# Optimization experiments

Hardware: AMD Instinct MI355X
Metric: run time of the kernel (lower is better)

Reference implementation:

```python
import jax, jax.numpy as jnp
import numpy as np

N, IN_DIM, HEADS, C = 100000, 128, 4, 32  # out_dim = HEADS*C = 128
E = 1600000


def setup_inputs() -> dict:
    key = jax.random.key(0)
    ks = jax.random.split(key, 9)
    x = jax.random.normal(ks[0], (N, IN_DIM), dtype=jnp.float32)
    edge_index = jax.random.randint(ks[1], (2, E), 0, N, dtype=jnp.int64)
    # GATConv params
    W = jax.random.normal(ks[2], (HEADS * C, IN_DIM), dtype=jnp.float32) * (1.0 / np.sqrt(IN_DIM))
    att_src = jax.random.normal(ks[3], (HEADS, C), dtype=jnp.float32) * 0.1
    att_dst = jax.random.normal(ks[4], (HEADS, C), dtype=jnp.float32) * 0.1
    bias = jax.random.normal(ks[5], (HEADS * C,), dtype=jnp.float32) * 0.01
    # complex phase + LayerNorm params
    phase = jax.random.normal(ks[6], (HEADS * C,), dtype=jnp.float32) * 0.02
    gamma = 1.0 + jax.random.normal(ks[7], (HEADS * C,), dtype=jnp.float32) * 0.01
    beta = jax.random.normal(ks[8], (HEADS * C,), dtype=jnp.float32) * 0.01
    return {"x": x, "edge_index": edge_index, "W": W, "att_src": att_src,
            "att_dst": att_dst, "bias": bias, "phase": phase, "gamma": gamma, "beta": beta}


def reference(x, edge_index, W, att_src, att_dst, bias, phase, gamma, beta):
    src, dst = edge_index[0], edge_index[1]
    h = (x @ W.T).reshape(N, HEADS, C)                      # [N,H,C]
    a_src = jnp.einsum('nhc,hc->nh', h, att_src)            # [N,H]
    a_dst = jnp.einsum('nhc,hc->nh', h, att_dst)
    e = jax.nn.leaky_relu(a_src[src] + a_dst[dst], 0.2)     # [E,H]
    # segment softmax over destination nodes (numerically stable)
    m = jax.ops.segment_max(e, dst, num_segments=N)         # [N,H]
    ex = jnp.exp(e - m[dst])
    s = jax.ops.segment_sum(ex, dst, num_segments=N)        # [N,H]
    alpha = ex / (s[dst] + 1e-16)                           # [E,H]
    msg = h[src] * alpha[:, :, None]                        # [E,H,C]
    out = jax.ops.segment_sum(msg, dst, num_segments=N).reshape(N, HEADS * C) + bias
    # complex phase magnitude: sqrt((h cos p)^2 + (h sin p)^2 + eps)
    mag = jnp.sqrt((out * jnp.cos(phase)) ** 2 + (out * jnp.sin(phase)) ** 2 + 1e-12)
    # LayerNorm
    mu = mag.mean(-1, keepdims=True)
    var = ((mag - mu) ** 2).mean(-1, keepdims=True)
    hn = (mag - mu) / jnp.sqrt(var + 1e-5) * gamma + beta
    return jax.nn.gelu(hn, approximate=False)
```

## Files before the change

### kernel.cpp

```cpp
#include <hip/hip_runtime.h>
#include <hip/hip_bf16.h>

#define N_ 100000
#define E_ 1600000
#define D_ 128
#define H_ 4
#define C_ 32
#define CAP 64
#define XSTR 136
#define NBUILD 256
#define NLIN 512

using bf16 = __hip_bfloat16;
typedef __attribute__((ext_vector_type(8))) short short8;
typedef __attribute__((ext_vector_type(4))) float f32x4;
typedef __attribute__((ext_vector_type(2))) float f32x2;

__device__ __forceinline__ float u2f(unsigned u) { return __uint_as_float(u); }
__device__ __forceinline__ unsigned short f2bu(float v) {
  bf16 t = __float2bfloat16(v);
  return *(unsigned short*)&t;
}

__global__ __launch_bounds__(256) void k_build_linear(
    const float* __restrict__ x, const float* __restrict__ W,
    const float* __restrict__ att_src, const float* __restrict__ att_dst,
    const int* __restrict__ ei, int* __restrict__ cnt, int* __restrict__ slot,
    bf16* __restrict__ h, float* __restrict__ a_src, float* __restrict__ a_dst) {
  __shared__ unsigned short WB[16384];
  __shared__ unsigned short XS[64 * XSTR];
  __shared__ float ats[128], atd[128];
  const int tid = threadIdx.x;
  const int bid = blockIdx.x;
  const int role = bid % 3;

  if (role == 0) {
    const int bb = bid / 3;
    for (int base = bb * 2048; base < E_; base += NBUILD * 2048) {
      int d[8], s[8];
      bool live[8];
#pragma unroll
      for (int k = 0; k < 8; k++) {
        const int e = base + k * 256 + tid;
        live[k] = e < E_;
        d[k] = 0; s[k] = 0;
        if (live[k]) { d[k] = ei[E_ + e]; s[k] = ei[e]; }
      }
#pragma unroll
      for (int k = 0; k < 8; k++) {
        if (live[k]) {
          const int p = atomicAdd(&cnt[d[k]], 1);
          if (p < CAP) slot[d[k] * CAP + p] = s[k];
        }
      }
    }
    return;
  }

  const int lb = (bid / 3) * 2 + (role - 1);
  const int lane = tid & 63, w = tid >> 6;
  const int n15 = lane & 15, quad = lane >> 4;

  for (int i = tid; i < 16384; i += 256) {
    const int n = i >> 7, k = i & 127;
    const int kk = k >> 5, q = (k >> 3) & 3, j = k & 7;
    const int frag = kk * 8 + (n >> 4);
    WB[frag * 512 + q * 128 + (n & 15) * 8 + j] = f2bu(W[n * 128 + k]);
  }
  if (tid < 128) { ats[tid] = att_src[tid]; atd[tid] = att_dst[tid]; }
  __syncthreads();

  const int nrb = (N_ + 63) / 64;
  for (int rb = lb; rb < nrb; rb += NLIN) {
    const int row0 = rb * 64;
    const int arow = row0 + w * 16 + n15;

    short8 af[4];
#pragma unroll
    for (int kk = 0; kk < 4; kk++) {
      float4 p = make_float4(0.f, 0.f, 0.f, 0.f);
      float4 q = make_float4(0.f, 0.f, 0.f, 0.f);
      if (arow < N_) {
        const float* xp = &x[(size_t)arow * 128 + kk * 32 + quad * 8];
        p = *(const float4*)xp;
        q = *(const float4*)(xp + 4);
      }
      short8 a;
      a[0] = f2bu(p.x); a[1] = f2bu(p.y); a[2] = f2bu(p.z); a[3] = f2bu(p.w);
      a[4] = f2bu(q.x); a[5] = f2bu(q.y); a[6] = f2bu(q.z); a[7] = f2bu(q.w);
      af[kk] = a;
    }

    f32x4 acc[8] = {};
#pragma unroll
    for (int kk = 0; kk < 4; kk++)
#pragma unroll
      for (int t = 0; t < 8; t++) {
        const short8 b = *(const short8*)&WB[(kk * 8 + t) * 512 + lane * 8];
        acc[t] = __builtin_amdgcn_mfma_f32_16x16x32_bf16(af[kk], b, acc[t], 0, 0, 0);
      }

#pragma unroll
    for (int t = 0; t < 8; t++)
#pragma unroll
      for (int reg = 0; reg < 4; reg++)
        XS[(w * 16 + quad * 4 + reg) * XSTR + t * 16 + n15] = f2bu(acc[t][reg]);

    const int lrow = lane >> 2, hd = lane & 3, cb = hd * 32;
    const int grow = row0 + w * 16 + lrow;
    if (grow < N_) {
      float ps = 0.f, pd = 0.f;
#pragma unroll
      for (int g = 0; g < 4; g++) {
        const uint4 v = *(const uint4*)&XS[(w * 16 + lrow) * XSTR + cb + g * 8];
        *(uint4*)&h[(size_t)grow * 128 + cb + g * 8] = v;
        const unsigned uu[4] = {v.x, v.y, v.z, v.w};
#pragma unroll
        for (int p2 = 0; p2 < 4; p2++) {
          const float f0 = u2f(uu[p2] << 16);
          const float f1 = u2f(uu[p2] & 0xffff0000u);
          const int cc = cb + g * 8 + p2 * 2;
          ps = fmaf(f0, ats[cc], ps);  ps = fmaf(f1, ats[cc + 1], ps);
          pd = fmaf(f0, atd[cc], pd);  pd = fmaf(f1, atd[cc + 1], pd);
        }
      }
      a_src[grow * 4 + hd] = ps;
      a_dst[grow * 4 + hd] = pd;
    }
  }
}

__global__ __launch_bounds__(256) void k_gather(
    const int* __restrict__ cnt, const int* __restrict__ slot,
    const float* __restrict__ a_src, const float* __restrict__ a_dst,
    const bf16* __restrict__ h, const float* __restrict__ bias,
    const float* __restrict__ gamma, const float* __restrict__ beta,
    float* __restrict__ out) {
  const int lane = threadIdx.x & 63;
  const int d = blockIdx.x * 4 + (threadIdx.x >> 6);
  if (d >= N_) return;
  const int head = lane >> 4;
  const int ch = lane * 2;
  const int deg0 = cnt[d];
  const int deg = deg0 < CAP ? deg0 : CAP;
  const float ad = a_dst[d * 4 + head];
  const int* __restrict__ srow = slot + (size_t)d * CAP;

  int my_src = 0;
  if (lane < deg) my_src = srow[lane];

  float acc0 = 0.f, acc1 = 0.f, sumw = 0.f;

  int j = 0;
  for (; j + 8 <= deg; j += 8) {
    int ss[8];
#pragma unroll
    for (int k = 0; k < 8; k++) ss[k] = __builtin_amdgcn_readlane(my_src, j + k);
    float as[8];
#pragma unroll
    for (int k = 0; k < 8; k++) as[k] = a_src[ss[k] * 4 + head];
    unsigned hh[8];
#pragma unroll
    for (int k = 0; k < 8; k++) hh[k] = *(const unsigned*)&h[((size_t)ss[k] << 7) + ch];
#pragma unroll
    for (int k = 0; k < 8; k++) {
      float ev = as[k] + ad;
      ev = (ev > 0.f) ? ev : 0.2f * ev;
      const float wv = __expf(ev);
      sumw += wv;
      acc0 = fmaf(wv, u2f(hh[k] << 16), acc0);
      acc1 = fmaf(wv, u2f(hh[k] & 0xffff0000u), acc1);
    }
  }
  for (; j + 4 <= deg; j += 4) {
    int ss[4];
#pragma unroll
    for (int k = 0; k < 4; k++) ss[k] = __builtin_amdgcn_readlane(my_src, j + k);
    float as[4];
#pragma unroll
    for (int k = 0; k < 4; k++) as[k] = a_src[ss[k] * 4 + head];
    unsigned hh[4];
#pragma unroll
    for (int k = 0; k < 4; k++) hh[k] = *(const unsigned*)&h[((size_t)ss[k] << 7) + ch];
#pragma unroll
    for (int k = 0; k < 4; k++) {
      float ev = as[k] + ad;
      ev = (ev > 0.f) ? ev : 0.2f * ev;
      const float wv = __expf(ev);
      sumw += wv;
      acc0 = fmaf(wv, u2f(hh[k] << 16), acc0);
      acc1 = fmaf(wv, u2f(hh[k] & 0xffff0000u), acc1);
    }
  }
  for (; j < deg; ++j) {
    const int s = __builtin_amdgcn_readlane(my_src, j);
    const float as = a_src[s * 4 + head];
    const unsigned hv = *(const unsigned*)&h[((size_t)s << 7) + ch];
    float ev = as + ad;
    ev = (ev > 0.f) ? ev : 0.2f * ev;
    const float wv = __expf(ev);
    sumw += wv;
    acc0 = fmaf(wv, u2f(hv << 16), acc0);
    acc1 = fmaf(wv, u2f(hv & 0xffff0000u), acc1);
  }

  const float inv = 1.0f / (sumw + 1e-16f);
  const float2 bi = *(const float2*)&bias[ch];
  const float v0 = acc0 * inv + bi.x;
  const float v1 = acc1 * inv + bi.y;
  const float m0i = sqrtf(v0 * v0 + 1e-12f);
  const float m1i = sqrtf(v1 * v1 + 1e-12f);

  float s1r = m0i + m1i;
#pragma unroll
  for (int off = 32; off > 0; off >>= 1) s1r += __shfl_xor(s1r, off);
  const float mu = s1r * (1.0f / 128.0f);
  const float d0 = m0i - mu, d1 = m1i - mu;
  float q = d0 * d0 + d1 * d1;
#pragma unroll
  for (int off = 32; off > 0; off >>= 1) q += __shfl_xor(q, off);
  const float rstd = rsqrtf(q * (1.0f / 128.0f) + 1e-5f);
  const float2 ga = *(const float2*)&gamma[ch];
  const float2 be = *(const float2*)&beta[ch];
  const float hn0 = d0 * rstd * ga.x + be.x;
  const float hn1 = d1 * rstd * ga.y + be.y;
  const float g0 = 0.5f * hn0 * (1.0f + erff(hn0 * 0.70710678118654752f));
  const float g1 = 0.5f * hn1 * (1.0f + erff(hn1 * 0.70710678118654752f));
  f32x2 gv; gv.x = g0; gv.y = g1;
  __builtin_nontemporal_store(gv, (f32x2*)&out[(size_t)d * 128 + ch]);
}

extern "C" void kernel_launch(void* const* d_in, const int* in_sizes, int n_in,
                              void* d_out, int out_size, void* d_ws, size_t ws_size,
                              hipStream_t stream) {
  const float* x       = (const float*)d_in[0];
  const int*   ei      = (const int*)d_in[1];
  const float* W       = (const float*)d_in[2];
  const float* att_src = (const float*)d_in[3];
  const float* att_dst = (const float*)d_in[4];
  const float* bias    = (const float*)d_in[5];
  const float* gamma   = (const float*)d_in[7];
  const float* beta    = (const float*)d_in[8];
  float* out = (float*)d_out;

  bf16*  h     = (bf16*)d_ws;
  float* a_src = (float*)(h + (size_t)N_ * D_);
  float* a_dst = a_src + (size_t)N_ * H_;
  int*   cnt   = (int*)(a_dst + (size_t)N_ * H_);
  int*   slot  = cnt + (size_t)N_;

  (void)hipMemsetAsync(cnt, 0, (size_t)N_ * sizeof(int), stream);

  k_build_linear<<<768, 256, 0, stream>>>(x, W, att_src, att_dst, ei, cnt,
                                          slot, h, a_src, a_dst);
  k_gather<<<(N_ + 3) / 4, 256, 0, stream>>>(cnt, slot, a_src, a_dst, h,
                                             bias, gamma, beta, out);
}
```

Before: 300.0 us.

## Replace per-node atomic slot lists with partitioned counting-sort CSR build

Replaces the global per-destination atomicAdd into fixed 64-slot lists with a two-level counting sort. Edges are histogrammed into 782 partitions of 128 nodes, scanned, and scattered with LDS atomics into packed (src, local dst) words. Each gather block then sorts its partition's edges in shared memory and handles 128 nodes, four waves doing 32 each. This removes the contended global atomics and the slot array, but adds two kernel launches, a single-block serial scan, and a fixed EBUF cap that silently truncates partitions with more than 2560 edges (about 2048 on average).

```diff
diff --git a/kernel.cpp b/kernel.cpp
--- a/kernel.cpp
+++ b/kernel.cpp
@@ -6,10 +6,13 @@
 #define D_ 128
 #define H_ 4
 #define C_ 32
-#define CAP 64
 #define XSTR 136
-#define NBUILD 256
-#define NLIN 512
+#define NSCAT 128
+#define E_CHUNK 12500
+#define PARTS 782
+#define NP 128
+#define EBUF 2560
+#define NLIN 640
 
 using bf16 = __hip_bfloat16;
 typedef __attribute__((ext_vector_type(8))) short short8;
@@ -22,42 +25,78 @@
   return *(unsigned short*)&t;
 }
 
-__global__ __launch_bounds__(256) void k_build_linear(
+__global__ __launch_bounds__(256) void k_histo(const int* __restrict__ ei,
+                                               int* __restrict__ count) {
+  __shared__ int hist[PARTS];
+  const int b = blockIdx.x, tid = threadIdx.x;
+  for (int i = tid; i < PARTS; i += 256) hist[i] = 0;
+  __syncthreads();
+  const int base = b * E_CHUNK;
+  for (int i = tid; i < E_CHUNK; i += 256) {
+    const int d = ei[E_ + base + i];
+    atomicAdd(&hist[d >> 7], 1);
+  }
+  __syncthreads();
+  for (int p = tid; p < PARTS; p += 256) count[p * NSCAT + b] = hist[p];
+}
+
+__global__ __launch_bounds__(1024) void k_scan(int* __restrict__ count,
+                                               int* __restrict__ part_ptr) {
+  __shared__ int ps[1024];
+  const int p = threadIdx.x;
+  int sum = 0;
+  if (p < PARTS)
+    for (int b = 0; b < NSCAT; b++) sum += count[p * NSCAT + b];
+  ps[p] = (p < PARTS) ? sum : 0;
+  __syncthreads();
+  for (int off = 1; off < 1024; off <<= 1) {
+    const int v = (p >= off) ? ps[p - off] : 0;
+    __syncthreads();
+    ps[p] += v;
+    __syncthreads();
+  }
+  if (p < PARTS) {
+    const int excl = ps[p] - sum;
+    part_ptr[p] = excl;
+    int run = excl;
+    for (int b = 0; b < NSCAT; b++) {
+      const int c = count[p * NSCAT + b];
+      count[p * NSCAT + b] = run;
+      run += c;
+    }
+  }
+  if (p == 0) part_ptr[PARTS] = E_;
+}
+
+__global__ __launch_bounds__(256) void k_scatter_linear(
     const float* __restrict__ x, const float* __restrict__ W,
     const float* __restrict__ att_src, const float* __restrict__ att_dst,
-    const int* __restrict__ ei, int* __restrict__ cnt, int* __restrict__ slot,
-    bf16* __restrict__ h, float* __restrict__ a_src, float* __restrict__ a_dst) {
+    const int* __restrict__ ei, const int* __restrict__ base,
+    int* __restrict__ eout, bf16* __restrict__ h,
+    float* __restrict__ a_src, float* __restrict__ a_dst) {
   __shared__ unsigned short WB[16384];
   __shared__ unsigned short XS[64 * XSTR];
   __shared__ float ats[128], atd[128];
   const int tid = threadIdx.x;
   const int bid = blockIdx.x;
-  const int role = bid % 3;
-
-  if (role == 0) {
-    const int bb = bid / 3;
-    for (int base = bb * 2048; base < E_; base += NBUILD * 2048) {
-      int d[8], s[8];
-      bool live[8];
-#pragma unroll
-      for (int k = 0; k < 8; k++) {
-        const int e = base + k * 256 + tid;
-        live[k] = e < E_;
-        d[k] = 0; s[k] = 0;
-        if (live[k]) { d[k] = ei[E_ + e]; s[k] = ei[e]; }
-      }
-#pragma unroll
-      for (int k = 0; k < 8; k++) {
-        if (live[k]) {
-          const int p = atomicAdd(&cnt[d[k]], 1);
-          if (p < CAP) slot[d[k] * CAP + p] = s[k];
-        }
-      }
+
+  if (bid < NSCAT) {
+    int* lbase = (int*)WB;
+    const int b = bid;
+    for (int p = tid; p < PARTS; p += 256) lbase[p] = base[p * NSCAT + b];
+    __syncthreads();
+    const int ebase = b * E_CHUNK;
+    for (int i = tid; i < E_CHUNK; i += 256) {
+      const int e = ebase + i;
+      const int s = ei[e];
+      const int d = ei[E_ + e];
+      const int pos = atomicAdd(&lbase[d >> 7], 1);
+      eout[pos] = s | ((d & 127) << 20);
     }
     return;
   }
 
-  const int lb = (bid / 3) * 2 + (role - 1);
+  const int lb = bid - NSCAT;
   const int lane = tid & 63, w = tid >> 6;
   const int n15 = lane & 15, quad = lane >> 4;
 
@@ -96,8 +135,8 @@
     for (int kk = 0; kk < 4; kk++)
 #pragma unroll
       for (int t = 0; t < 8; t++) {
-        const short8 b = *(const short8*)&WB[(kk * 8 + t) * 512 + lane * 8];
-        acc[t] = __builtin_amdgcn_mfma_f32_16x16x32_bf16(af[kk], b, acc[t], 0, 0, 0);
+        const short8 bfr = *(const short8*)&WB[(kk * 8 + t) * 512 + lane * 8];
+        acc[t] = __builtin_amdgcn_mfma_f32_16x16x32_bf16(af[kk], bfr, acc[t], 0, 0, 0);
       }
 
 #pragma unroll
@@ -131,103 +170,113 @@
 }
 
 __global__ __launch_bounds__(256) void k_gather(
-    const int* __restrict__ cnt, const int* __restrict__ slot,
+    const int* __restrict__ part_ptr, const int* __restrict__ eout,
     const float* __restrict__ a_src, const float* __restrict__ a_dst,
     const bf16* __restrict__ h, const float* __restrict__ bias,
     const float* __restrict__ gamma, const float* __restrict__ beta,
     float* __restrict__ out) {
-  const int lane = threadIdx.x & 63;
-  const int d = blockIdx.x * 4 + (threadIdx.x >> 6);
-  if (d >= N_) return;
+  __shared__ int ebuf[EBUF];
+  __shared__ int lsrc[EBUF];
+  __shared__ int lcnt[NP], loff[NP], lptr[NP], ls[NP];
+  const int p = blockIdx.x, tid = threadIdx.x;
+  const int lo = part_ptr[p];
+  int ne = part_ptr[p + 1] - lo;
+  if (ne > EBUF) ne = EBUF;
+
+  for (int i = tid; i < ne; i += 256) ebuf[i] = eout[lo + i];
+  for (int n = tid; n < NP; n += 256) { lcnt[n] = 0; loff[n] = 0; }
+  __syncthreads();
+  for (int i = tid; i < ne; i += 256) atomicAdd(&lcnt[ebuf[i] >> 20], 1);
+  __syncthreads();
+  if (tid < NP) ls[tid] = lcnt[tid];
+  __syncthreads();
+  for (int off = 1; off < NP; off <<= 1) {
+    const int v = (tid < NP && tid >= off) ? ls[tid - off] : 0;
+    __syncthreads();
+    if (tid < NP) ls[tid] += v;
+    __syncthreads();
+  }
+  if (tid < NP) lptr[tid] = ls[tid] - lcnt[tid];
+  __syncthreads();
+  for (int i = tid; i < ne; i += 256) {
+    const int v = ebuf[i];
+    const int n = v >> 20;
+    const int off = atomicAdd(&loff[n], 1);
+    lsrc[lptr[n] + off] = v & 0x1FFFF;
+  }
+  __syncthreads();
+
+  const int lane = tid & 63, wid = tid >> 6;
   const int head = lane >> 4;
   const int ch = lane * 2;
-  const int deg0 = cnt[d];
-  const int deg = deg0 < CAP ? deg0 : CAP;
-  const float ad = a_dst[d * 4 + head];
-  const int* __restrict__ srow = slot + (size_t)d * CAP;
-
-  int my_src = 0;
-  if (lane < deg) my_src = srow[lane];
-
-  float acc0 = 0.f, acc1 = 0.f, sumw = 0.f;
-
-  int j = 0;
-  for (; j + 8 <= deg; j += 8) {
-    int ss[8];
-#pragma unroll
-    for (int k = 0; k < 8; k++) ss[k] = __builtin_amdgcn_readlane(my_src, j + k);
-    float as[8];
-#pragma unroll
-    for (int k = 0; k < 8; k++) as[k] = a_src[ss[k] * 4 + head];
-    unsigned hh[8];
-#pragma unroll
-    for (int k = 0; k < 8; k++) hh[k] = *(const unsigned*)&h[((size_t)ss[k] << 7) + ch];
-#pragma unroll
-    for (int k = 0; k < 8; k++) {
-      float ev = as[k] + ad;
+
+  for (int nn = 0; nn < 32; nn++) {
+    const int n = wid * 32 + nn;
+    const int g = p * NP + n;
+    if (g >= N_) break;
+    const int deg = lcnt[n];
+    const int p0 = lptr[n];
+    const float ad = a_dst[g * 4 + head];
+    float acc0 = 0.f, acc1 = 0.f, sumw = 0.f;
+
+    int j = 0;
+    for (; j + 8 <= deg; j += 8) {
+      int ss[8];
+#pragma unroll
+      for (int k = 0; k < 8; k++) ss[k] = lsrc[p0 + j + k];
+      float as[8];
+#pragma unroll
+      for (int k = 0; k < 8; k++) as[k] = a_src[ss[k] * 4 + head];
+      unsigned hh[8];
+#pragma unroll
+      for (int k = 0; k < 8; k++) hh[k] = *(const unsigned*)&h[((size_t)ss[k] << 7) + ch];
+#pragma unroll
+      for (int k = 0; k < 8; k++) {
+        float ev = as[k] + ad;
+        ev = (ev > 0.f) ? ev : 0.2f * ev;
+        const float wv = __expf(ev);
+        sumw += wv;
+        acc0 = fmaf(wv, u2f(hh[k] << 16), acc0);
+        acc1 = fmaf(wv, u2f(hh[k] & 0xffff0000u), acc1);
+      }
+    }
+    for (; j < deg; ++j) {
+      const int s = lsrc[p0 + j];
+      const float as = a_src[s * 4 + head];
+      const unsigned hv = *(const unsigned*)&h[((size_t)s << 7) + ch];
+      float ev = as + ad;
       ev = (ev > 0.f) ? ev : 0.2f * ev;
       const float wv = __expf(ev);
       sumw += wv;
-      acc0 = fmaf(wv, u2f(hh[k] << 16), acc0);
-      acc1 = fmaf(wv, u2f(hh[k] & 0xffff0000u), acc1);
-    }
-  }
-  for (; j + 4 <= deg; j += 4) {
-    int ss[4];
-#pragma unroll
-    for (int k = 0; k < 4; k++) ss[k] = __builtin_amdgcn_readlane(my_src, j + k);
-    float as[4];
-#pragma unroll
-    for (int k = 0; k < 4; k++) as[k] = a_src[ss[k] * 4 + head];
-    unsigned hh[4];
-#pragma unroll
-    for (int k = 0; k < 4; k++) hh[k] = *(const unsigned*)&h[((size_t)ss[k] << 7) + ch];
-#pragma unroll
-    for (int k = 0; k < 4; k++) {
-      float ev = as[k] + ad;
-      ev = (ev > 0.f) ? ev : 0.2f * ev;
-      const float wv = __expf(ev);
-      sumw += wv;
-      acc0 = fmaf(wv, u2f(hh[k] << 16), acc0);
-      acc1 = fmaf(wv, u2f(hh[k] & 0xffff0000u), acc1);
-    }
-  }
-  for (; j < deg; ++j) {
-    const int s = __builtin_amdgcn_readlane(my_src, j);
-    const float as = a_src[s * 4 + head];
-    const unsigned hv = *(const unsigned*)&h[((size_t)s << 7) + ch];
-    float ev = as + ad;
-    ev = (ev > 0.f) ? ev : 0.2f * ev;
-    const float wv = __expf(ev);
-    sumw += wv;
-    acc0 = fmaf(wv, u2f(hv << 16), acc0);
-    acc1 = fmaf(wv, u2f(hv & 0xffff0000u), acc1);
-  }
-
-  const float inv = 1.0f / (sumw + 1e-16f);
-  const float2 bi = *(const float2*)&bias[ch];
-  const float v0 = acc0 * inv + bi.x;
-  const float v1 = acc1 * inv + bi.y;
-  const float m0i = sqrtf(v0 * v0 + 1e-12f);
-  const float m1i = sqrtf(v1 * v1 + 1e-12f);
-
-  float s1r = m0i + m1i;
-#pragma unroll
-  for (int off = 32; off > 0; off >>= 1) s1r += __shfl_xor(s1r, off);
-  const float mu = s1r * (1.0f / 128.0f);
-  const float d0 = m0i - mu, d1 = m1i - mu;
-  float q = d0 * d0 + d1 * d1;
-#pragma unroll
-  for (int off = 32; off > 0; off >>= 1) q += __shfl_xor(q, off);
-  const float rstd = rsqrtf(q * (1.0f / 128.0f) + 1e-5f);
-  const float2 ga = *(const float2*)&gamma[ch];
-  const float2 be = *(const float2*)&beta[ch];
-  const float hn0 = d0 * rstd * ga.x + be.x;
-  const float hn1 = d1 * rstd * ga.y + be.y;
-  const float g0 = 0.5f * hn0 * (1.0f + erff(hn0 * 0.70710678118654752f));
-  const float g1 = 0.5f * hn1 * (1.0f + erff(hn1 * 0.70710678118654752f));
-  f32x2 gv; gv.x = g0; gv.y = g1;
-  __builtin_nontemporal_store(gv, (f32x2*)&out[(size_t)d * 128 + ch]);
+      acc0 = fmaf(wv, u2f(hv << 16), acc0);
+      acc1 = fmaf(wv, u2f(hv & 0xffff0000u), acc1);
+    }
+
+    const float inv = 1.0f / (sumw + 1e-16f);
+    const float2 bi = *(const float2*)&bias[ch];
+    const float v0 = acc0 * inv + bi.x;
+    const float v1 = acc1 * inv + bi.y;
+    const float m0i = sqrtf(v0 * v0 + 1e-12f);
+    const float m1i = sqrtf(v1 * v1 + 1e-12f);
+
+    float s1r = m0i + m1i;
+#pragma unroll
+    for (int off = 32; off > 0; off >>= 1) s1r += __shfl_xor(s1r, off);
+    const float mu = s1r * (1.0f / 128.0f);
+    const float d0 = m0i - mu, d1 = m1i - mu;
+    float q = d0 * d0 + d1 * d1;
+#pragma unroll
+    for (int off = 32; off > 0; off >>= 1) q += __shfl_xor(q, off);
+    const float rstd = rsqrtf(q * (1.0f / 128.0f) + 1e-5f);
+    const float2 ga = *(const float2*)&gamma[ch];
+    const float2 be = *(const float2*)&beta[ch];
+    const float hn0 = d0 * rstd * ga.x + be.x;
+    const float hn1 = d1 * rstd * ga.y + be.y;
+    const float g0 = 0.5f * hn0 * (1.0f + erff(hn0 * 0.70710678118654752f));
+    const float g1 = 0.5f * hn1 * (1.0f + erff(hn1 * 0.70710678118654752f));
+    f32x2 gv; gv.x = g0; gv.y = g1;
+    __builtin_nontemporal_store(gv, (f32x2*)&out[(size_t)g * 128 + ch]);
+  }
 }
 
 extern "C" void kernel_launch(void* const* d_in, const int* in_sizes, int n_in,
@@ -243,16 +292,18 @@
   const float* beta    = (const float*)d_in[8];
   float* out = (float*)d_out;
 
-  bf16*  h     = (bf16*)d_ws;
-  float* a_src = (float*)(h + (size_t)N_ * D_);
-  float* a_dst = a_src + (size_t)N_ * H_;
-  int*   cnt   = (int*)(a_dst + (size_t)N_ * H_);
-  int*   slot  = cnt + (size_t)N_;
-
-  (void)hipMemsetAsync(cnt, 0, (size_t)N_ * sizeof(int), stream);
-
-  k_build_linear<<<768, 256, 0, stream>>>(x, W, att_src, att_dst, ei, cnt,
-                                          slot, h, a_src, a_dst);
-  k_gather<<<(N_ + 3) / 4, 256, 0, stream>>>(cnt, slot, a_src, a_dst, h,
-                                             bias, gamma, beta, out);
-}
+  bf16*  h        = (bf16*)d_ws;
+  float* a_src    = (float*)(h + (size_t)N_ * D_);
+  float* a_dst    = a_src + (size_t)N_ * H_;
+  int*   count    = (int*)(a_dst + (size_t)N_ * H_);
+  int*   part_ptr = count + 784 * NSCAT;
+  int*   eout     = part_ptr + 800;
+
+  k_histo<<<NSCAT, 256, 0, stream>>>(ei, count);
+  k_scan<<<1, 1024, 0, stream>>>(count, part_ptr);
+  k_scatter_linear<<<NSCAT + NLIN, 256, 0, stream>>>(x, W, att_src, att_dst,
+                                                     ei, count, eout, h,
+                                                     a_src, a_dst);
+  k_gather<<<PARTS, 256, 0, stream>>>(part_ptr, eout, a_src, a_dst, h,
+                                      bias, gamma, beta, out);
+}
```

Result: slower. 361.7 us (+20.6%).
